# Optimization experiments

Hardware: AMD Instinct MI355X
Metric: run time of the kernel (lower is better)

Reference implementation:

```python
import jax, jax.numpy as jnp
import numpy as np

H = 256          # hidden_dim
D = 64           # dim_dynamic
R = 49           # pooler_resolution ** 2
N = 2000         # bs * num_proposals
EPS = 1e-5


def _ln(x, g, b):
    m = jnp.mean(x, axis=-1, keepdims=True)
    v = jnp.mean(jnp.square(x - m), axis=-1, keepdims=True)
    return (x - m) * jax.lax.rsqrt(v + EPS) * g + b


def setup_inputs() -> dict:
    key = jax.random.key(0)
    ks = jax.random.split(key, 6)
    pro_features = jax.random.normal(ks[0], (1, N, H), dtype=jnp.float32)
    roi_features = jax.random.normal(ks[1], (R, N, H), dtype=jnp.float32)
    # dynamic_layer: Linear(H, num_dynamic * H * D) with num_dynamic = 2
    W_dyn = jax.random.normal(ks[2], (H, 2 * H * D), dtype=jnp.float32) * 0.02
    b_dyn = jnp.zeros((2 * H * D,), dtype=jnp.float32)
    # out_layer: Linear(H * R, H)
    W_out = jax.random.normal(ks[3], (H * R, H), dtype=jnp.float32) * 0.02
    b_out = jnp.zeros((H,), dtype=jnp.float32)
    g1 = jnp.ones((D,), dtype=jnp.float32); b1 = jnp.zeros((D,), dtype=jnp.float32)
    g2 = jnp.ones((H,), dtype=jnp.float32); b2 = jnp.zeros((H,), dtype=jnp.float32)
    g3 = jnp.ones((H,), dtype=jnp.float32); b3 = jnp.zeros((H,), dtype=jnp.float32)
    return {"pro_features": pro_features, "roi_features": roi_features,
            "W_dyn": W_dyn, "b_dyn": b_dyn, "W_out": W_out, "b_out": b_out,
            "g1": g1, "b1": b1, "g2": g2, "b2": b2, "g3": g3, "b3": b3}


def reference(pro_features, roi_features, W_dyn, b_dyn, W_out, b_out,
              g1, b1, g2, b2, g3, b3):
    # roi_features: (R, N, H) -> features: (N, R, H)
    feats = jnp.transpose(roi_features, (1, 0, 2))
    # per-instance dynamic parameters: (N, 2*H*D)
    params = pro_features[0] @ W_dyn + b_dyn
    num_params = H * D
    p1 = params[:, :num_params].reshape(-1, H, D)   # (N, H, D)
    p2 = params[:, num_params:].reshape(-1, D, H)   # (N, D, H)
    f = jnp.einsum('nrh,nhd->nrd', feats, p1)       # bmm 1
    f = jax.nn.relu(_ln(f, g1, b1))
    f = jnp.einsum('nrd,ndh->nrh', f, p2)           # bmm 2
    f = jax.nn.relu(_ln(f, g2, b2))
    f = f.reshape(f.shape[0], R * H)                # flatten(1)
    f = jax.nn.relu(_ln(f @ W_out + b_out, g3, b3))
    return f  # (N, H)
```

## Files before the change

kernel.cpp:

```cpp
#include <hip/hip_runtime.h>

typedef unsigned short u16;
typedef __attribute__((ext_vector_type(8))) short short8;
typedef __attribute__((ext_vector_type(4))) float f32x4;

#define N_INST 2000
#define H_DIM 256
#define D_DIM 64
#define R_DIM 49
#define LN_EPS 1e-5f
#define SPLITK 14

__device__ __forceinline__ u16 f2bf(float f) {
  union { float f; unsigned int i; } x; x.f = f;
  unsigned int r = x.i + 0x7fffu + ((x.i >> 16) & 1u);
  return (u16)(r >> 16);
}
__device__ __forceinline__ float bf2f(u16 u) {
  union { unsigned int i; float f; } x; x.i = ((unsigned int)u) << 16; return x.f;
}
__device__ __forceinline__ short8 ld8(const u16* p) {
  return *reinterpret_cast<const short8*>(p);
}
__device__ __forceinline__ short8 pack8(float4 a, float4 b) {
  short8 r;
  r[0] = (short)f2bf(a.x); r[1] = (short)f2bf(a.y);
  r[2] = (short)f2bf(a.z); r[3] = (short)f2bf(a.w);
  r[4] = (short)f2bf(b.x); r[5] = (short)f2bf(b.y);
  r[6] = (short)f2bf(b.z); r[7] = (short)f2bf(b.w);
  return r;
}
__device__ __forceinline__ f32x4 mfma16(short8 a, short8 b, f32x4 c) {
  return __builtin_amdgcn_mfma_f32_16x16x32_bf16(a, b, c, 0, 0, 0);
}
__device__ __forceinline__ void wave_reduce2(float& s, float& s2) {
#pragma unroll
  for (int off = 32; off > 0; off >>= 1) {
    s  += __shfl_down(s, off);
    s2 += __shfl_down(s2, off);
  }
  s = __shfl(s, 0); s2 = __shfl(s2, 0);
}
__device__ __forceinline__ void gload16(const u16* g, u16* l) {
  __builtin_amdgcn_global_load_lds(
      (const __attribute__((address_space(1))) void*)g,
      (__attribute__((address_space(3))) void*)l, 16, 0, 0);
}

__global__ __launch_bounds__(256) void cast_pro(const float* __restrict__ in,
                                                u16* __restrict__ out, int n4) {
  for (int i = blockIdx.x * 256 + threadIdx.x; i < n4; i += gridDim.x * 256) {
    float4 v = ((const float4*)in)[i];
    u16* op = out + i * 4;
    op[0] = f2bf(v.x); op[1] = f2bf(v.y); op[2] = f2bf(v.z); op[3] = f2bf(v.w);
  }
}

__global__ __launch_bounds__(256) void cast_wdyn(const float* __restrict__ W,
                                                 u16* __restrict__ WT) {
  __shared__ u16 T[64][65];
  const int tid = threadIdx.x;
  const int wave = tid >> 6, lane = tid & 63;
  const int half = blockIdx.x >> 10;
  const int b = blockIdx.x & 1023;
  const int kt = b >> 8;
  long colbase, rowbase; int rstride;
  if (half == 0) {
    int h = b & 255;
    colbase = (long)h * 64; rowbase = h; rstride = 256;
  } else {
    int d = b & 63, hc = (b >> 6) & 3;
    colbase = 16384L + d * 256 + hc * 64;
    rowbase = 16384L + hc * 4096 + d; rstride = 64;
  }
#pragma unroll
  for (int i = 0; i < 16; ++i) {
    int kk = wave * 16 + i;
    int k = kt * 64 + kk;
    T[kk][lane] = f2bf(W[(long)k * 32768 + colbase + lane]);
  }
  __syncthreads();
#pragma unroll
  for (int i = 0; i < 16; ++i) {
    int jj = wave * 16 + i;
    long ro = rowbase + (long)jj * rstride;
    WT[ro * 256 + kt * 64 + lane] = T[lane][jj];
  }
}

__global__ __launch_bounds__(256) void cast_wout(const float* __restrict__ W,
                                                 u16* __restrict__ WT) {
  __shared__ u16 T[64][65];
  const int tid = threadIdx.x;
  const int wave = tid >> 6, lane = tid & 63;
  const int kt = blockIdx.x >> 2, ct = blockIdx.x & 3;
#pragma unroll
  for (int i = 0; i < 16; ++i) {
    int kk = wave * 16 + i;
    long k = (long)kt * 64 + kk;
    T[kk][lane] = f2bf(W[k * 256 + ct * 64 + lane]);
  }
  __syncthreads();
#pragma unroll
  for (int i = 0; i < 16; ++i) {
    int cc = wave * 16 + i;
    long c = (long)ct * 64 + cc;
    WT[c * 12544 + (long)kt * 64 + lane] = T[lane][cc];
  }
}

__global__ __launch_bounds__(256, 3) void gemm128(
    const u16* __restrict__ A, int lda, int M,
    const u16* __restrict__ BT, int ldbt,
    const float* __restrict__ bias, int bias_mode,
    void* __restrict__ Cout, int ldc, long c_stride_s,
    int ksteps, int n_blocks, int out_f32)
{
  union Smem {
    struct { u16 a[2][128 * 32]; u16 b[2][128 * 32]; } s;
    u16 cb[128 * 128];
  };
  __shared__ Smem sm;

  const int tid = threadIdx.x;
  const int wave = tid >> 6, lane = tid & 63;
  const int quad = lane >> 4, l16 = lane & 15;
  const int wm = wave >> 1, wn = wave & 1;
  const int bid = blockIdx.x;
  const int mblk = bid / n_blocks, nblk = bid - mblk * n_blocks;
  const int m0 = mblk * 128, n0 = nblk * 128;
  const int s = blockIdx.y;
  const int kb = s * ksteps * 32;

  const int cl = tid & 3;
  const int r0 = tid >> 2, r1 = 64 + (tid >> 2);
  const int cg0 = cl ^ ((r0 >> 1) & 3);
  const int cg1 = cl ^ ((r1 >> 1) & 3);
  int ga0 = m0 + r0; if (ga0 >= M) ga0 = M - 1;
  int ga1 = m0 + r1; if (ga1 >= M) ga1 = M - 1;
  const u16* gA0 = A + (long)ga0 * lda + kb + cg0 * 8;
  const u16* gA1 = A + (long)ga1 * lda + kb + cg1 * 8;
  const u16* gB0 = BT + (long)(n0 + r0) * ldbt + kb + cg0 * 8;
  const u16* gB1 = BT + (long)(n0 + r1) * ldbt + kb + cg1 * 8;

  int fAoff[4], fBoff[4];
#pragma unroll
  for (int i = 0; i < 4; ++i) {
    int rt = wm * 64 + i * 16 + l16;
    fAoff[i] = rt * 32 + (quad ^ ((rt >> 1) & 3)) * 8;
    int ct = wn * 64 + i * 16 + l16;
    fBoff[i] = ct * 32 + (quad ^ ((ct >> 1) & 3)) * 8;
  }

  f32x4 acc[4][4];
#pragma unroll
  for (int mi = 0; mi < 4; ++mi)
#pragma unroll
    for (int ni = 0; ni < 4; ++ni) acc[mi][ni] = f32x4{0.f, 0.f, 0.f, 0.f};

  gload16(gA0, &sm.s.a[0][tid * 8]);
  gload16(gA1, &sm.s.a[0][(tid + 256) * 8]);
  gload16(gB0, &sm.s.b[0][tid * 8]);
  gload16(gB1, &sm.s.b[0][(tid + 256) * 8]);

  for (int ks = 0; ks < ksteps; ++ks) {
    const int cur = ks & 1, nxt = cur ^ 1;
    __syncthreads();
    if (ks + 1 < ksteps) {
      const int ko = (ks + 1) * 32;
      gload16(gA0 + ko, &sm.s.a[nxt][tid * 8]);
      gload16(gA1 + ko, &sm.s.a[nxt][(tid + 256) * 8]);
      gload16(gB0 + ko, &sm.s.b[nxt][tid * 8]);
      gload16(gB1 + ko, &sm.s.b[nxt][(tid + 256) * 8]);
    }
    short8 av[4], bv[4];
#pragma unroll
    for (int i = 0; i < 4; ++i) {
      av[i] = ld8(&sm.s.a[cur][fAoff[i]]);
      bv[i] = ld8(&sm.s.b[cur][fBoff[i]]);
    }
#pragma unroll
    for (int mi = 0; mi < 4; ++mi)
#pragma unroll
      for (int ni = 0; ni < 4; ++ni)
        acc[mi][ni] = mfma16(av[mi], bv[ni], acc[mi][ni]);
  }

  if (!out_f32) {
    float bvv[4];
#pragma unroll
    for (int ni = 0; ni < 4; ++ni) {
      int col = n0 + wn * 64 + ni * 16 + l16;
      int bi = col;
      if (bias_mode == 3)
        bi = (col < 16384) ? (((col & 255) << 6) + (col >> 8))
                           : (16384 + ((col & 63) << 8) + ((col >> 6) & 255));
      bvv[ni] = bias ? bias[bi] : 0.f;
    }
    __syncthreads();
#pragma unroll
    for (int mi = 0; mi < 4; ++mi)
#pragma unroll
      for (int ni = 0; ni < 4; ++ni)
#pragma unroll
        for (int i = 0; i < 4; ++i) {
          int row = wm * 64 + mi * 16 + quad * 4 + i;
          int col = wn * 64 + ni * 16 + l16;
          sm.cb[row * 128 + col] = f2bf(acc[mi][ni][i] + bvv[ni]);
        }
    __syncthreads();
    u16* Cp = (u16*)Cout;
#pragma unroll
    for (int j = 0; j < 8; ++j) {
      int lin = j * 2048 + tid * 8;
      int row = lin >> 7, col = lin & 127;
      int grow = m0 + row;
      if (grow < M)
        *reinterpret_cast<short8*>(Cp + (long)grow * ldc + n0 + col) =
            ld8(&sm.cb[lin]);
    }
  } else {
    float* Cp = (float*)Cout + (long)s * c_stride_s;
#pragma unroll
    for (int mi = 0; mi < 4; ++mi)
#pragma unroll
      for (int ni = 0; ni < 4; ++ni) {
        int col = n0 + wn * 64 + ni * 16 + l16;
#pragma unroll
        for (int i = 0; i < 4; ++i) {
          int row = m0 + wm * 64 + mi * 16 + quad * 4 + i;
          if (row < M) Cp[(long)row * ldc + col] = acc[mi][ni][i];
        }
      }
  }
}

__global__ __launch_bounds__(256, 4) void bmm12_ln(
    const float* __restrict__ roi,
    const u16* __restrict__ P12,
    const float* __restrict__ g1, const float* __restrict__ b1,
    const float* __restrict__ g2, const float* __restrict__ b2,
    u16* __restrict__ f2n)
{
  __shared__ __align__(16) u16 p1b[16384];
  __shared__ __align__(16) u16 f1b[4096];
  const int n = blockIdx.x;
  const int tid = threadIdx.x;
  const int wave = tid >> 6, lane = tid & 63;
  const int quad = lane >> 4, l16 = lane & 15;
  const int wstripe = wave * 16;

  const u16* P1n = P12 + (long)n * 32768;
#pragma unroll
  for (int j = 0; j < 8; ++j) {
    int lc = j * 256 + tid;
    int d = lc >> 5, c = lc & 31;
    int cg = (c & 24) | ((c & 7) ^ (d & 7));
    gload16(P1n + d * 256 + cg * 8, &p1b[lc * 8]);
  }
  int r = wstripe + l16;
  int rr = (r < R_DIM) ? r : 0;
  const float* Arow = roi + ((long)rr * N_INST + n) * H_DIM + quad * 8;
  short8 sa[8];
#pragma unroll
  for (int ks = 0; ks < 8; ++ks) {
    float4 va = ((const float4*)(Arow + ks * 32))[0];
    float4 vb = ((const float4*)(Arow + ks * 32))[1];
    sa[ks] = pack8(va, vb);
  }
  const u16* P2n = P12 + (long)n * 32768 + 16384;
  short8 pf[4][2];
#pragma unroll
  for (int hs = 0; hs < 4; ++hs)
#pragma unroll
    for (int ks = 0; ks < 2; ++ks) {
      int h = wave * 64 + hs * 16 + l16;
      pf[hs][ks] = ld8(P2n + h * 64 + (ks * 4 + quad) * 8);
    }
  float gv1[4], bv1[4];
#pragma unroll
  for (int sub = 0; sub < 4; ++sub) {
    gv1[sub] = g1[sub * 16 + l16]; bv1[sub] = b1[sub * 16 + l16];
  }
  __syncthreads();

  f32x4 acc1[4];
#pragma unroll
  for (int i = 0; i < 4; ++i) acc1[i] = f32x4{0.f, 0.f, 0.f, 0.f};
#pragma unroll
  for (int ks = 0; ks < 8; ++ks) {
#pragma unroll
    for (int sub = 0; sub < 4; ++sub) {
      int d = sub * 16 + l16;
      int q = ks * 4 + quad;
      int c = (q & 24) | ((q & 7) ^ (d & 7));
      acc1[sub] = mfma16(sa[ks], ld8(&p1b[d * 256 + c * 8]), acc1[sub]);
    }
  }

  {
    float s1[4], s2[4];
#pragma unroll
    for (int i = 0; i < 4; ++i) {
      s1[i] = 0.f; s2[i] = 0.f;
#pragma unroll
      for (int sub = 0; sub < 4; ++sub) {
        float v = acc1[sub][i]; s1[i] += v; s2[i] += v * v;
      }
    }
#pragma unroll
    for (int m = 1; m < 16; m <<= 1)
#pragma unroll
      for (int i = 0; i < 4; ++i) {
        s1[i] += __shfl_xor(s1[i], m, 16);
        s2[i] += __shfl_xor(s2[i], m, 16);
      }
#pragma unroll
    for (int i = 0; i < 4; ++i) {
      float mean = s1[i] * (1.f / 64.f);
      float var = s2[i] * (1.f / 64.f) - mean * mean;
      float rs = rsqrtf(var + LN_EPS);
      int row = wstripe + quad * 4 + i;
#pragma unroll
      for (int sub = 0; sub < 4; ++sub) {
        float y = fmaxf((acc1[sub][i] - mean) * rs * gv1[sub] + bv1[sub], 0.f);
        int kc = (sub * 2 + (l16 >> 3)) ^ (row & 7);
        f1b[row * 64 + kc * 8 + (l16 & 7)] = f2bf(y);
      }
    }
  }
  __syncthreads();

  f32x4 acc2[4][4];
#pragma unroll
  for (int rs = 0; rs < 4; ++rs)
#pragma unroll
    for (int hs = 0; hs < 4; ++hs) acc2[rs][hs] = f32x4{0.f, 0.f, 0.f, 0.f};
#pragma unroll
  for (int ks = 0; ks < 2; ++ks) {
#pragma unroll
    for (int rs = 0; rs < 4; ++rs) {
      int row = rs * 16 + l16;
      int c2 = (ks * 4 + quad) ^ (row & 7);
      short8 af = ld8(&f1b[row * 64 + c2 * 8]);
#pragma unroll
      for (int hs = 0; hs < 4; ++hs)
        acc2[rs][hs] = mfma16(af, pf[hs][ks], acc2[rs][hs]);
    }
  }

  float s1[4][4], s2[4][4];
#pragma unroll
  for (int rs = 0; rs < 4; ++rs)
#pragma unroll
    for (int i = 0; i < 4; ++i) {
      float a = 0.f, b = 0.f;
#pragma unroll
      for (int hs = 0; hs < 4; ++hs) {
        float v = acc2[rs][hs][i]; a += v; b += v * v;
      }
      s1[rs][i] = a; s2[rs][i] = b;
    }
#pragma unroll
  for (int m = 1; m < 16; m <<= 1)
#pragma unroll
    for (int rs = 0; rs < 4; ++rs)
#pragma unroll
      for (int i = 0; i < 4; ++i) {
        s1[rs][i] += __shfl_xor(s1[rs][i], m, 16);
        s2[rs][i] += __shfl_xor(s2[rs][i], m, 16);
      }
  float2* lnst = reinterpret_cast<float2*>(&p1b[14336]);
  if (l16 == 0) {
#pragma unroll
    for (int rs = 0; rs < 4; ++rs)
#pragma unroll
      for (int i = 0; i < 4; ++i) {
        int row = rs * 16 + quad * 4 + i;
        lnst[row * 4 + wave] = float2{s1[rs][i], s2[rs][i]};
      }
  }
  __syncthreads();

#pragma unroll
  for (int rs = 0; rs < 4; ++rs)
#pragma unroll
    for (int i = 0; i < 4; ++i) {
      int row = rs * 16 + quad * 4 + i;
      f32x4 qa = *reinterpret_cast<const f32x4*>(&lnst[row * 4]);
      f32x4 qb = *reinterpret_cast<const f32x4*>(&lnst[row * 4 + 2]);
      float S1 = qa[0] + qa[2] + qb[0] + qb[2];
      float S2 = qa[1] + qa[3] + qb[1] + qb[3];
      float mean = S1 * (1.f / 256.f);
      float var = S2 * (1.f / 256.f) - mean * mean;
      float rsq = rsqrtf(var + LN_EPS);
      if (row < R_DIM) {
#pragma unroll
        for (int hs = 0; hs < 4; ++hs)
          p1b[row * 264 + wave * 64 + hs * 16 + l16] =
              f2bf((acc2[rs][hs][i] - mean) * rsq);
      }
    }
  __syncthreads();

  u16* f2out = f2n + (long)n * (R_DIM * H_DIM);
  for (int t = tid; t < R_DIM * 32; t += 256) {
    int row = t >> 5, c = t & 31;
    short8 z8 = ld8(&p1b[row * 264 + c * 8]);
    const float4* gp = (const float4*)(g2 + c * 8);
    const float4* bp = (const float4*)(b2 + c * 8);
    float4 ga = gp[0], gb = gp[1], ba = bp[0], bb = bp[1];
    short8 y;
    y[0] = (short)f2bf(fmaxf(bf2f((u16)z8[0]) * ga.x + ba.x, 0.f));
    y[1] = (short)f2bf(fmaxf(bf2f((u16)z8[1]) * ga.y + ba.y, 0.f));
    y[2] = (short)f2bf(fmaxf(bf2f((u16)z8[2]) * ga.z + ba.z, 0.f));
    y[3] = (short)f2bf(fmaxf(bf2f((u16)z8[3]) * ga.w + ba.w, 0.f));
    y[4] = (short)f2bf(fmaxf(bf2f((u16)z8[4]) * gb.x + bb.x, 0.f));
    y[5] = (short)f2bf(fmaxf(bf2f((u16)z8[5]) * gb.y + bb.y, 0.f));
    y[6] = (short)f2bf(fmaxf(bf2f((u16)z8[6]) * gb.z + bb.z, 0.f));
    y[7] = (short)f2bf(fmaxf(bf2f((u16)z8[7]) * gb.w + bb.w, 0.f));
    *reinterpret_cast<short8*>(f2out + row * 256 + c * 8) = y;
  }
}

__global__ __launch_bounds__(64) void ln3_k(
    const float* __restrict__ partial,
    const float* __restrict__ b_out,
    const float* __restrict__ g3, const float* __restrict__ b3,
    float* __restrict__ out)
{
  const int n = blockIdx.x;
  const int lane = threadIdx.x;
  float x[4], sv = 0.f, s2 = 0.f;
#pragma unroll
  for (int j = 0; j < 4; ++j) {
    int h = lane + 64 * j;
    float v = b_out[h];
#pragma unroll
    for (int ss = 0; ss < SPLITK; ++ss)
      v += partial[((long)ss * N_INST + n) * H_DIM + h];
    x[j] = v; sv += v; s2 += v * v;
  }
  wave_reduce2(sv, s2);
  float mean = sv * (1.f / 256.f);
  float var = s2 * (1.f / 256.f) - mean * mean;
  float rs = rsqrtf(var + LN_EPS);
#pragma unroll
  for (int j = 0; j < 4; ++j) {
    int h = lane + 64 * j;
    float y = fmaxf((x[j] - mean) * rs * g3[h] + b3[h], 0.f);
    out[(long)n * H_DIM + h] = y;
  }
}

extern "C" void kernel_launch(void* const* d_in, const int* in_sizes, int n_in,
                              void* d_out, int out_size, void* d_ws, size_t ws_size,
                              hipStream_t stream) {
  const float* pro  = (const float*)d_in[0];
  const float* roi  = (const float*)d_in[1];
  const float* Wdyn = (const float*)d_in[2];
  const float* bdyn = (const float*)d_in[3];
  const float* Wout = (const float*)d_in[4];
  const float* bout = (const float*)d_in[5];
  const float* g1 = (const float*)d_in[6];
  const float* b1 = (const float*)d_in[7];
  const float* g2 = (const float*)d_in[8];
  const float* b2 = (const float*)d_in[9];
  const float* g3 = (const float*)d_in[10];
  const float* b3 = (const float*)d_in[11];
  float* out = (float*)d_out;

  char* ws = (char*)d_ws;
  u16* proB  = (u16*)ws;
  u16* WdynT = (u16*)(ws + 1024000);
  u16* WoutT = (u16*)(ws + 17801216);
  u16* P12   = (u16*)(ws + 24223744);
  u16* f2n   = (u16*)(ws + 155295744);
  float* partial = (float*)(ws + 24223744);

  dim3 blk(256);

  cast_pro<<<dim3(500), blk, 0, stream>>>(pro, proB, 512000 / 4);
  cast_wdyn<<<dim3(2048), blk, 0, stream>>>(Wdyn, WdynT);
  cast_wout<<<dim3(784), blk, 0, stream>>>(Wout, WoutT);

  gemm128<<<dim3(16 * 256, 1), blk, 0, stream>>>(
      proB, H_DIM, N_INST, WdynT, H_DIM, bdyn, 3,
      (void*)P12, 32768, 0L, 8, 256, 0);
  bmm12_ln<<<dim3(N_INST), blk, 0, stream>>>(roi, P12, g1, b1, g2, b2, f2n);
  gemm128<<<dim3(16 * 2, SPLITK), blk, 0, stream>>>(
      f2n, R_DIM * H_DIM, N_INST, WoutT, R_DIM * H_DIM, nullptr, 0,
      (void*)partial, H_DIM, (long)N_INST * H_DIM, 28, 2, 1);
  ln3_k<<<dim3(N_INST), dim3(64), 0, stream>>>(partial, bout, g3, b3, out);
}
```

Before: 326.4 us.

## Deepen GEMM prefetch pipeline, merge prep casts, vectorize final layernorm

The GEMM now uses a 5-slot LDS ring, keeps three stages of global-to-LDS loads in flight, and waits with explicit vmcnt counts plus a raw barrier instead of a full syncthreads each step. Occupancy drops from 3 to 2 blocks per CU because of the larger LDS footprint. The three cast/transpose kernels are merged into one launch to cut launch overhead. The final split-K reduction plus layernorm packs 8 rows per block and uses float4 loads with 32-lane shuffles. Risks are lower occupancy and the correctness of the hand-counted vmcnt waits.

Result: no change. 330.9 us (+1.4%).

```diff
diff --git a/kernel.cpp b/kernel.cpp
--- a/kernel.cpp
+++ b/kernel.cpp
@@ -10,6 +10,7 @@
 #define R_DIM 49
 #define LN_EPS 1e-5f
 #define SPLITK 14
+#define NBUF 5
 
 __device__ __forceinline__ u16 f2bf(float f) {
   union { float f; unsigned int i; } x; x.f = f;
@@ -33,83 +34,73 @@
 __device__ __forceinline__ f32x4 mfma16(short8 a, short8 b, f32x4 c) {
   return __builtin_amdgcn_mfma_f32_16x16x32_bf16(a, b, c, 0, 0, 0);
 }
-__device__ __forceinline__ void wave_reduce2(float& s, float& s2) {
-#pragma unroll
-  for (int off = 32; off > 0; off >>= 1) {
-    s  += __shfl_down(s, off);
-    s2 += __shfl_down(s2, off);
-  }
-  s = __shfl(s, 0); s2 = __shfl(s2, 0);
-}
 __device__ __forceinline__ void gload16(const u16* g, u16* l) {
   __builtin_amdgcn_global_load_lds(
       (const __attribute__((address_space(1))) void*)g,
       (__attribute__((address_space(3))) void*)l, 16, 0, 0);
 }
 
-__global__ __launch_bounds__(256) void cast_pro(const float* __restrict__ in,
-                                                u16* __restrict__ out, int n4) {
-  for (int i = blockIdx.x * 256 + threadIdx.x; i < n4; i += gridDim.x * 256) {
-    float4 v = ((const float4*)in)[i];
-    u16* op = out + i * 4;
-    op[0] = f2bf(v.x); op[1] = f2bf(v.y); op[2] = f2bf(v.z); op[3] = f2bf(v.w);
-  }
-}
-
-__global__ __launch_bounds__(256) void cast_wdyn(const float* __restrict__ W,
-                                                 u16* __restrict__ WT) {
+__global__ __launch_bounds__(256) void prep_all(
+    const float* __restrict__ pro,  u16* __restrict__ proB,
+    const float* __restrict__ Wdyn, u16* __restrict__ WdynT,
+    const float* __restrict__ Wout, u16* __restrict__ WoutT) {
   __shared__ u16 T[64][65];
   const int tid = threadIdx.x;
   const int wave = tid >> 6, lane = tid & 63;
-  const int half = blockIdx.x >> 10;
-  const int b = blockIdx.x & 1023;
-  const int kt = b >> 8;
-  long colbase, rowbase; int rstride;
-  if (half == 0) {
-    int h = b & 255;
-    colbase = (long)h * 64; rowbase = h; rstride = 256;
+  const int b = blockIdx.x;
+  if (b < 2048) {
+    const int half = b >> 10;
+    const int bb = b & 1023;
+    const int kt = bb >> 8;
+    long colbase, rowbase; int rstride;
+    if (half == 0) {
+      int h = bb & 255;
+      colbase = (long)h * 64; rowbase = h; rstride = 256;
+    } else {
+      int d = bb & 63, hc = (bb >> 6) & 3;
+      colbase = 16384L + d * 256 + hc * 64;
+      rowbase = 16384L + hc * 4096 + d; rstride = 64;
+    }
+#pragma unroll
+    for (int i = 0; i < 16; ++i) {
+      int kk = wave * 16 + i;
+      int k = kt * 64 + kk;
+      T[kk][lane] = f2bf(Wdyn[(long)k * 32768 + colbase + lane]);
+    }
+    __syncthreads();
+#pragma unroll
+    for (int i = 0; i < 16; ++i) {
+      int jj = wave * 16 + i;
+      long ro = rowbase + (long)jj * rstride;
+      WdynT[ro * 256 + kt * 64 + lane] = T[lane][jj];
+    }
+  } else if (b < 2832) {
+    const int b2 = b - 2048;
+    const int kt = b2 >> 2, ct = b2 & 3;
+#pragma unroll
+    for (int i = 0; i < 16; ++i) {
+      int kk = wave * 16 + i;
+      long k = (long)kt * 64 + kk;
+      T[kk][lane] = f2bf(Wout[k * 256 + ct * 64 + lane]);
+    }
+    __syncthreads();
+#pragma unroll
+    for (int i = 0; i < 16; ++i) {
+      int cc = wave * 16 + i;
+      long c = (long)ct * 64 + cc;
+      WoutT[c * 12544 + (long)kt * 64 + lane] = T[lane][cc];
+    }
   } else {
-    int d = b & 63, hc = (b >> 6) & 3;
-    colbase = 16384L + d * 256 + hc * 64;
-    rowbase = 16384L + hc * 4096 + d; rstride = 64;
-  }
-#pragma unroll
-  for (int i = 0; i < 16; ++i) {
-    int kk = wave * 16 + i;
-    int k = kt * 64 + kk;
-    T[kk][lane] = f2bf(W[(long)k * 32768 + colbase + lane]);
-  }
-  __syncthreads();
-#pragma unroll
-  for (int i = 0; i < 16; ++i) {
-    int jj = wave * 16 + i;
-    long ro = rowbase + (long)jj * rstride;
-    WT[ro * 256 + kt * 64 + lane] = T[lane][jj];
-  }
-}
-
-__global__ __launch_bounds__(256) void cast_wout(const float* __restrict__ W,
-                                                 u16* __restrict__ WT) {
-  __shared__ u16 T[64][65];
-  const int tid = threadIdx.x;
-  const int wave = tid >> 6, lane = tid & 63;
-  const int kt = blockIdx.x >> 2, ct = blockIdx.x & 3;
-#pragma unroll
-  for (int i = 0; i < 16; ++i) {
-    int kk = wave * 16 + i;
-    long k = (long)kt * 64 + kk;
-    T[kk][lane] = f2bf(W[k * 256 + ct * 64 + lane]);
-  }
-  __syncthreads();
-#pragma unroll
-  for (int i = 0; i < 16; ++i) {
-    int cc = wave * 16 + i;
-    long c = (long)ct * 64 + cc;
-    WT[c * 12544 + (long)kt * 64 + lane] = T[lane][cc];
-  }
-}
-
-__global__ __launch_bounds__(256, 3) void gemm128(
+    const int n4 = 128000;
+    for (int i = (b - 2832) * 256 + tid; i < n4; i += 500 * 256) {
+      float4 v = ((const float4*)pro)[i];
+      u16* op = proB + i * 4;
+      op[0] = f2bf(v.x); op[1] = f2bf(v.y); op[2] = f2bf(v.z); op[3] = f2bf(v.w);
+    }
+  }
+}
+
+__global__ __launch_bounds__(256, 2) void gemm128(
     const u16* __restrict__ A, int lda, int M,
     const u16* __restrict__ BT, int ldbt,
     const float* __restrict__ bias, int bias_mode,
@@ -117,7 +108,7 @@
     int ksteps, int n_blocks, int out_f32)
 {
   union Smem {
-    struct { u16 a[2][128 * 32]; u16 b[2][128 * 32]; } s;
+    struct { u16 a[NBUF][128 * 32]; u16 b[NBUF][128 * 32]; } s;
     u16 cb[128 * 128];
   };
   __shared__ Smem sm;
@@ -158,35 +149,44 @@
 #pragma unroll
     for (int ni = 0; ni < 4; ++ni) acc[mi][ni] = f32x4{0.f, 0.f, 0.f, 0.f};
 
-  gload16(gA0, &sm.s.a[0][tid * 8]);
-  gload16(gA1, &sm.s.a[0][(tid + 256) * 8]);
-  gload16(gB0, &sm.s.b[0][tid * 8]);
-  gload16(gB1, &sm.s.b[0][(tid + 256) * 8]);
+  auto stage = [&](int slot, int kg) {
+    const int ko = kg * 32;
+    gload16(gA0 + ko, &sm.s.a[slot][tid * 8]);
+    gload16(gA1 + ko, &sm.s.a[slot][(tid + 256) * 8]);
+    gload16(gB0 + ko, &sm.s.b[slot][tid * 8]);
+    gload16(gB1 + ko, &sm.s.b[slot][(tid + 256) * 8]);
+  };
+
+  stage(0, 0); stage(1, 1); stage(2, 2);
+  int sk = 3, ssl = 3, sc = 0;
 
   for (int ks = 0; ks < ksteps; ++ks) {
-    const int cur = ks & 1, nxt = cur ^ 1;
-    __syncthreads();
-    if (ks + 1 < ksteps) {
-      const int ko = (ks + 1) * 32;
-      gload16(gA0 + ko, &sm.s.a[nxt][tid * 8]);
-      gload16(gA1 + ko, &sm.s.a[nxt][(tid + 256) * 8]);
-      gload16(gB0 + ko, &sm.s.b[nxt][tid * 8]);
-      gload16(gB1 + ko, &sm.s.b[nxt][(tid + 256) * 8]);
-    }
+    if (sk < ksteps) {
+      stage(ssl, sk);
+      ++sk; if (++ssl == NBUF) ssl = 0;
+    }
+    const int rem = (sk - ks - 1) * 4;
+    if (rem >= 12)     asm volatile("s_waitcnt vmcnt(12)" ::: "memory");
+    else if (rem == 8) asm volatile("s_waitcnt vmcnt(8)" ::: "memory");
+    else if (rem == 4) asm volatile("s_waitcnt vmcnt(4)" ::: "memory");
+    else               asm volatile("s_waitcnt vmcnt(0)" ::: "memory");
+    __builtin_amdgcn_s_barrier();
     short8 av[4], bv[4];
 #pragma unroll
     for (int i = 0; i < 4; ++i) {
-      av[i] = ld8(&sm.s.a[cur][fAoff[i]]);
-      bv[i] = ld8(&sm.s.b[cur][fBoff[i]]);
+      av[i] = ld8(&sm.s.a[sc][fAoff[i]]);
+      bv[i] = ld8(&sm.s.b[sc][fBoff[i]]);
     }
 #pragma unroll
     for (int mi = 0; mi < 4; ++mi)
 #pragma unroll
       for (int ni = 0; ni < 4; ++ni)
         acc[mi][ni] = mfma16(av[mi], bv[ni], acc[mi][ni]);
+    if (++sc == NBUF) sc = 0;
   }
 
   if (!out_f32) {
+    __syncthreads();
     float bvv[4];
 #pragma unroll
     for (int ni = 0; ni < 4; ++ni) {
@@ -197,7 +197,6 @@
                            : (16384 + ((col & 63) << 8) + ((col >> 6) & 255));
       bvv[ni] = bias ? bias[bi] : 0.f;
     }
-    __syncthreads();
 #pragma unroll
     for (int mi = 0; mi < 4; ++mi)
 #pragma unroll
@@ -423,34 +422,52 @@
   }
 }
 
-__global__ __launch_bounds__(64) void ln3_k(
+__global__ __launch_bounds__(256) void ln3_k(
     const float* __restrict__ partial,
     const float* __restrict__ b_out,
     const float* __restrict__ g3, const float* __restrict__ b3,
     float* __restrict__ out)
 {
-  const int n = blockIdx.x;
-  const int lane = threadIdx.x;
-  float x[4], sv = 0.f, s2 = 0.f;
-#pragma unroll
-  for (int j = 0; j < 4; ++j) {
-    int h = lane + 64 * j;
-    float v = b_out[h];
-#pragma unroll
-    for (int ss = 0; ss < SPLITK; ++ss)
-      v += partial[((long)ss * N_INST + n) * H_DIM + h];
-    x[j] = v; sv += v; s2 += v * v;
-  }
-  wave_reduce2(sv, s2);
+  const int n = blockIdx.x * 8 + (threadIdx.x >> 5);
+  const int t = threadIdx.x & 31;
+  const int h0 = t * 8;
+  float4 xa = ((const float4*)(b_out + h0))[0];
+  float4 xb = ((const float4*)(b_out + h0))[1];
+#pragma unroll
+  for (int ss = 0; ss < SPLITK; ++ss) {
+    const float* pp = partial + ((long)ss * N_INST + n) * H_DIM + h0;
+    float4 va = ((const float4*)pp)[0];
+    float4 vb = ((const float4*)pp)[1];
+    xa.x += va.x; xa.y += va.y; xa.z += va.z; xa.w += va.w;
+    xb.x += vb.x; xb.y += vb.y; xb.z += vb.z; xb.w += vb.w;
+  }
+  float sv = xa.x + xa.y + xa.z + xa.w + xb.x + xb.y + xb.z + xb.w;
+  float s2 = xa.x * xa.x + xa.y * xa.y + xa.z * xa.z + xa.w * xa.w +
+             xb.x * xb.x + xb.y * xb.y + xb.z * xb.z + xb.w * xb.w;
+#pragma unroll
+  for (int m = 1; m < 32; m <<= 1) {
+    sv += __shfl_xor(sv, m, 32);
+    s2 += __shfl_xor(s2, m, 32);
+  }
   float mean = sv * (1.f / 256.f);
   float var = s2 * (1.f / 256.f) - mean * mean;
   float rs = rsqrtf(var + LN_EPS);
-#pragma unroll
-  for (int j = 0; j < 4; ++j) {
-    int h = lane + 64 * j;
-    float y = fmaxf((x[j] - mean) * rs * g3[h] + b3[h], 0.f);
-    out[(long)n * H_DIM + h] = y;
-  }
+  float4 ga = ((const float4*)(g3 + h0))[0];
+  float4 gb = ((const float4*)(g3 + h0))[1];
+  float4 ba = ((const float4*)(b3 + h0))[0];
+  float4 bb = ((const float4*)(b3 + h0))[1];
+  float4 ya, yb;
+  ya.x = fmaxf((xa.x - mean) * rs * ga.x + ba.x, 0.f);
+  ya.y = fmaxf((xa.y - mean) * rs * ga.y + ba.y, 0.f);
+  ya.z = fmaxf((xa.z - mean) * rs * ga.z + ba.z, 0.f);
+  ya.w = fmaxf((xa.w - mean) * rs * ga.w + ba.w, 0.f);
+  yb.x = fmaxf((xb.x - mean) * rs * gb.x + bb.x, 0.f);
+  yb.y = fmaxf((xb.y - mean) * rs * gb.y + bb.y, 0.f);
+  yb.z = fmaxf((xb.z - mean) * rs * gb.z + bb.z, 0.f);
+  yb.w = fmaxf((xb.w - mean) * rs * gb.w + bb.w, 0.f);
+  float* op = out + (long)n * H_DIM + h0;
+  ((float4*)op)[0] = ya;
+  ((float4*)op)[1] = yb;
 }
 
 extern "C" void kernel_launch(void* const* d_in, const int* in_sizes, int n_in,
@@ -480,16 +497,17 @@
 
   dim3 blk(256);
 
-  cast_pro<<<dim3(500), blk, 0, stream>>>(pro, proB, 512000 / 4);
-  cast_wdyn<<<dim3(2048), blk, 0, stream>>>(Wdyn, WdynT);
-  cast_wout<<<dim3(784), blk, 0, stream>>>(Wout, WoutT);
+  prep_all<<<dim3(3332), blk, 0, stream>>>(pro, proB, Wdyn, WdynT, Wout, WoutT);
 
   gemm128<<<dim3(16 * 256, 1), blk, 0, stream>>>(
       proB, H_DIM, N_INST, WdynT, H_DIM, bdyn, 3,
       (void*)P12, 32768, 0L, 8, 256, 0);
+
   bmm12_ln<<<dim3(N_INST), blk, 0, stream>>>(roi, P12, g1, b1, g2, b2, f2n);
+
   gemm128<<<dim3(16 * 2, SPLITK), blk, 0, stream>>>(
       f2n, R_DIM * H_DIM, N_INST, WoutT, R_DIM * H_DIM, nullptr, 0,
       (void*)partial, H_DIM, (long)N_INST * H_DIM, 28, 2, 1);
-  ln3_k<<<dim3(N_INST), dim3(64), 0, stream>>>(partial, bout, g3, b3, out);
-}
+
+  ln3_k<<<dim3(250), blk, 0, stream>>>(partial, bout, g3, b3, out);
+}
```
